# Optimization experiments

Hardware: AMD Instinct MI355X
Metric: run time of the kernel (lower is better)

## Reference

```python
import jax, jax.numpy as jnp
import numpy as np

EMBED = 1024
HEADS = 16
HEAD_DIM = EMBED // HEADS
EPS = 1e-5


def setup_inputs() -> dict:
    key = jax.random.key(0)
    ks = jax.random.split(key, 5)
    s = 1.0 / np.sqrt(EMBED)
    return {
        "x": jax.random.normal(ks[0], (2, 2048, EMBED), dtype=jnp.float32),
        "Wq": jax.random.normal(ks[1], (EMBED, EMBED), dtype=jnp.float32) * s,
        "Wk": jax.random.normal(ks[2], (EMBED, EMBED), dtype=jnp.float32) * s,
        "Wv": jax.random.normal(ks[3], (EMBED, EMBED), dtype=jnp.float32) * s,
        "Wout": jax.random.normal(ks[4], (EMBED, EMBED), dtype=jnp.float32) * s,
        "gamma": jnp.ones((EMBED,), dtype=jnp.float32),
        "beta": jnp.zeros((EMBED,), dtype=jnp.float32),
    }


def reference(x, Wq, Wk, Wv, Wout, gamma, beta):
    B, S, E = x.shape
    # nn.Linear(bias=False): y = x @ W.T; weight stored as [out, in]
    q = (x @ Wq.T).reshape(B, S, HEADS, HEAD_DIM)
    k = (x @ Wk.T).reshape(B, S, HEADS, HEAD_DIM)
    v = (x @ Wv.T).reshape(B, S, HEADS, HEAD_DIM)
    scale = 1.0 / jnp.sqrt(jnp.float32(HEAD_DIM)).astype(x.dtype)
    scores = jnp.einsum("bqhd,bkhd->bhqk", q, k) * scale  # [B,H,S,S]
    probs = jax.nn.softmax(scores, axis=-1)
    attn = jnp.einsum("bhqk,bkhd->bqhd", probs, v).reshape(B, S, E)
    out = attn @ Wout.T
    y = out + x
    mu = jnp.mean(y, axis=-1, keepdims=True)
    var = jnp.var(y, axis=-1, keepdims=True)
    return (y - mu) * jax.lax.rsqrt(var + EPS) * gamma + beta
```

## Files before the change

kernel.cpp:

```cpp
#include <hip/hip_runtime.h>
#include <hip/hip_bf16.h>
#include <cstdint>
#include <cstddef>

#define SEQ   2048
#define BATCH 2
#define NROWS 4096
#define EMB   1024
#define NHEAD 16
#define HD    64
#define KVBLK 64
#define NTG   16

typedef __attribute__((ext_vector_type(8))) short bf16x8;
typedef __attribute__((ext_vector_type(4))) float f32x4;
typedef __attribute__((ext_vector_type(16))) float f32x16;
typedef __attribute__((ext_vector_type(2))) int i32x2;
typedef __hip_bfloat16 bf16_t;

__device__ __forceinline__ int swz(int row, int cb) { return cb ^ ((row & 7) << 4); }

__device__ __forceinline__ void plswap(int a, int b, int& ra, int& rb) {
#if __has_builtin(__builtin_amdgcn_permlane32_swap)
  i32x2 r = __builtin_amdgcn_permlane32_swap(a, b, false, false);
  ra = r[0]; rb = r[1];
#else
  const int pa = __shfl_xor(a, 32), pb = __shfl_xor(b, 32);
  const bool lo = (threadIdx.x & 63) < 32;
  ra = lo ? a : pb;
  rb = lo ? pa : b;
#endif
}
__device__ __forceinline__ float pairmax32(float v) {
  int r0, r1;
  plswap(__float_as_int(v), __float_as_int(v), r0, r1);
  return fmaxf(__int_as_float(r0), __int_as_float(r1));
}
__device__ __forceinline__ float pairsum32(float v) {
  int r0, r1;
  plswap(__float_as_int(v), __float_as_int(v), r0, r1);
  return __int_as_float(r0) + __int_as_float(r1);
}

__global__ __launch_bounds__(256) void cast_f32_to_bf16(const float* __restrict__ in,
                                                        bf16_t* __restrict__ out, int n4) {
  int i = blockIdx.x * 256 + threadIdx.x;
  if (i >= n4) return;
  float4 v = reinterpret_cast<const float4*>(in)[i];
  union { ushort4 u; bf16_t h[4]; } o;
  o.h[0] = __float2bfloat16(v.x);
  o.h[1] = __float2bfloat16(v.y);
  o.h[2] = __float2bfloat16(v.z);
  o.h[3] = __float2bfloat16(v.w);
  reinterpret_cast<ushort4*>(out)[i] = o.u;
}

__global__ __launch_bounds__(256) void cast4_w(const float* __restrict__ a,
                                               const float* __restrict__ b,
                                               const float* __restrict__ c,
                                               const float* __restrict__ d,
                                               bf16_t* __restrict__ oa, bf16_t* __restrict__ ob,
                                               bf16_t* __restrict__ oc, bf16_t* __restrict__ od,
                                               int n4) {
  const int z = blockIdx.z;
  const float* in = (z == 0) ? a : (z == 1) ? b : (z == 2) ? c : d;
  bf16_t* out = (z == 0) ? oa : (z == 1) ? ob : (z == 2) ? oc : od;
  int i = blockIdx.x * 256 + threadIdx.x;
  if (i >= n4) return;
  float4 v = reinterpret_cast<const float4*>(in)[i];
  union { ushort4 u; bf16_t h[4]; } o;
  o.h[0] = __float2bfloat16(v.x);
  o.h[1] = __float2bfloat16(v.y);
  o.h[2] = __float2bfloat16(v.z);
  o.h[3] = __float2bfloat16(v.w);
  reinterpret_cast<ushort4*>(out)[i] = o.u;
}

template <int MODE>
__device__ __forceinline__ void gemm128_body(const bf16_t* __restrict__ A,
                                             const bf16_t* __restrict__ W,
                                             bf16_t* __restrict__ Ob,
                                             float* __restrict__ Of,
                                             const float* __restrict__ Res) {
  __shared__ __align__(16) bf16_t As[128 * 32];
  __shared__ __align__(16) bf16_t Bs[128 * 32];
  const int tid = threadIdx.x;
  const int lane = tid & 63;
  const int wv = tid >> 6;
  const int wm = wv >> 1, wn = wv & 1;
  const int brow = blockIdx.y * 128;
  const int bcol = blockIdx.x * 128;
  const int lr = lane & 15, lg = lane >> 4;

  f32x4 acc[4][4] = {};

  auto* As3 = (__attribute__((address_space(3))) char*)As;
  auto* Bs3 = (__attribute__((address_space(3))) char*)Bs;

  for (int k0 = 0; k0 < EMB; k0 += 32) {
    __syncthreads();
#pragma unroll
    for (int i = 0; i < 2; ++i) {
      const int chunk = i * 256 + tid;
      const int row = chunk >> 2;
      const int kc = (chunk & 3) * 8;
      const bf16_t* ga = A + (size_t)(brow + row) * EMB + k0 + kc;
      const bf16_t* gb = W + (size_t)(bcol + row) * EMB + k0 + kc;
      __builtin_amdgcn_global_load_lds((const __attribute__((address_space(1))) void*)ga,
                                       (__attribute__((address_space(3))) void*)(As3 + chunk * 16),
                                       16, 0, 0);
      __builtin_amdgcn_global_load_lds((const __attribute__((address_space(1))) void*)gb,
                                       (__attribute__((address_space(3))) void*)(Bs3 + chunk * 16),
                                       16, 0, 0);
    }
    __syncthreads();

    bf16x8 af[4], bfr[4];
#pragma unroll
    for (int m = 0; m < 4; ++m)
      af[m] = *reinterpret_cast<const bf16x8*>(&As[(wm * 64 + m * 16 + lr) * 32 + lg * 8]);
#pragma unroll
    for (int n = 0; n < 4; ++n)
      bfr[n] = *reinterpret_cast<const bf16x8*>(&Bs[(wn * 64 + n * 16 + lr) * 32 + lg * 8]);
#pragma unroll
    for (int m = 0; m < 4; ++m)
#pragma unroll
      for (int n = 0; n < 4; ++n)
        acc[m][n] = __builtin_amdgcn_mfma_f32_16x16x32_bf16(af[m], bfr[n], acc[m][n], 0, 0, 0);
  }

  const int r0 = brow + wm * 64;
  const int c0 = bcol + wn * 64;
#pragma unroll
  for (int m = 0; m < 4; ++m)
#pragma unroll
    for (int n = 0; n < 4; ++n) {
      if (MODE == 2) {
        const int row0 = r0 + m * 16 + lg * 4;
        const int col = c0 + n * 16 + lr;
        const size_t vt_row = (size_t)(row0 >> 11) * 1024 + col;
        const int s = row0 & 2047;
        union { uint2 u2; bf16_t h[4]; } pu;
#pragma unroll
        for (int r = 0; r < 4; ++r) pu.h[r] = __float2bfloat16(acc[m][n][r]);
        *reinterpret_cast<uint2*>(Ob + vt_row * SEQ + s) = pu.u2;
      } else {
#pragma unroll
        for (int r = 0; r < 4; ++r) {
          const int row = r0 + m * 16 + lg * 4 + r;
          const int col = c0 + n * 16 + lr;
          const size_t idx = (size_t)row * EMB + col;
          if (MODE == 0) Ob[idx] = __float2bfloat16(acc[m][n][r]);
          else Of[idx] = acc[m][n][r] + Res[idx];
        }
      }
    }
}

__global__ __launch_bounds__(256) void gemm_qkv(const bf16_t* __restrict__ X,
                                                const bf16_t* __restrict__ Wq,
                                                const bf16_t* __restrict__ Wk,
                                                const bf16_t* __restrict__ Wv,
                                                bf16_t* __restrict__ Q,
                                                bf16_t* __restrict__ K,
                                                bf16_t* __restrict__ Vt) {
  if (blockIdx.z == 0)      gemm128_body<0>(X, Wq, Q, nullptr, nullptr);
  else if (blockIdx.z == 1) gemm128_body<0>(X, Wk, K, nullptr, nullptr);
  else                      gemm128_body<2>(X, Wv, Vt, nullptr, nullptr);
}

__global__ __launch_bounds__(256) void gemm_out(const bf16_t* __restrict__ Attn,
                                                const bf16_t* __restrict__ Wo,
                                                float* __restrict__ Y,
                                                const float* __restrict__ X) {
  gemm128_body<1>(Attn, Wo, nullptr, Y, X);
}

__global__ __launch_bounds__(512, 4) void attn_kernel(const bf16_t* __restrict__ Q,
                                                      const bf16_t* __restrict__ K,
                                                      const bf16_t* __restrict__ Vt,
                                                      bf16_t* __restrict__ Oout) {
  __shared__ __align__(16) char L[65536];

  const int tid = threadIdx.x;
  const int lane = tid & 63;
  const int wv = tid >> 6;
  const int w = wv & 3;
  const int sg = wv >> 2;
  const int lq = lane & 31;
  const int lh = lane >> 5;

  const int f = blockIdx.x + 16 * blockIdx.y + 256 * blockIdx.z;
  const int ww = (f & 7) * 64 + (f >> 3);
  const int qb = ww & 15;
  const int h = (ww >> 4) & 15;
  const int b = ww >> 8;

  const size_t baseRow = (size_t)b * SEQ;
  const int hoff = h * HD;
  const int q0 = qb * 128 + w * 32;

  const float qscale = 0.125f * 1.44269504f;
  bf16x8 qf[4];
#pragma unroll
  for (int ks = 0; ks < 4; ++ks) {
    bf16x8 t = *reinterpret_cast<const bf16x8*>(
        &Q[(baseRow + q0 + lq) * EMB + hoff + ks * 16 + lh * 8]);
    union { bf16x8 v; bf16_t h[8]; } u;
    u.v = t;
#pragma unroll
    for (int e = 0; e < 8; ++e)
      u.h[e] = __float2bfloat16(__bfloat162float(u.h[e]) * qscale);
    qf[ks] = u.v;
  }

  f32x16 o0 = {}, o1 = {};
  float mrow = -1e30f, lrow = 0.f;

  auto* L3 = (__attribute__((address_space(3))) char*)L;
  const int gbase = sg * 32768;

  const int stid = tid & 255;
  const int srow = stid >> 3;
  const int scb = swz(srow, (stid & 7) * 16) >> 1;
  const bf16_t* kp = K + (baseRow + sg * 1024 + srow) * EMB + hoff + scb;
  const bf16_t* vp = Vt + ((size_t)(b * 1024 + hoff) + srow) * SEQ + sg * 1024 + scb;

  auto stage = [&](int buf) {
#pragma unroll
    for (int i = 0; i < 2; ++i) {
      const int c = i * 256 + stid;
      __builtin_amdgcn_global_load_lds(
          (const __attribute__((address_space(1))) void*)(kp + i * 32 * EMB),
          (__attribute__((address_space(3))) void*)(L3 + gbase + buf * 8192 + c * 16), 16, 0, 0);
      __builtin_amdgcn_global_load_lds(
          (const __attribute__((address_space(1))) void*)(vp + i * 32 * SEQ),
          (__attribute__((address_space(3))) void*)(L3 + gbase + 16384 + buf * 8192 + c * 16), 16, 0, 0);
    }
    kp += KVBLK * EMB;
    vp += KVBLK;
  };

  stage(0);
  __syncthreads();

  for (int t = 0; t < NTG; ++t) {
    const int cur = t & 1;
    if (t + 1 < NTG) stage(cur ^ 1);

    const char* Kb = (const char*)L + gbase + cur * 8192;
    const char* Vb = (const char*)L + gbase + 16384 + cur * 8192;

    f32x16 st0 = {}, st1 = {};
    __builtin_amdgcn_s_setprio(1);
#pragma unroll
    for (int ks = 0; ks < 4; ++ks) {
      bf16x8 kf0 = *reinterpret_cast<const bf16x8*>(Kb + lq * 128 + swz(lq, ks * 32 + lh * 16));
      st0 = __builtin_amdgcn_mfma_f32_32x32x16_bf16(kf0, qf[ks], st0, 0, 0, 0);
    }
#pragma unroll
    for (int ks = 0; ks < 4; ++ks) {
      bf16x8 kf1 = *reinterpret_cast<const bf16x8*>(Kb + (32 + lq) * 128 + swz(lq, ks * 32 + lh * 16));
      st1 = __builtin_amdgcn_mfma_f32_32x32x16_bf16(kf1, qf[ks], st1, 0, 0, 0);
    }
    __builtin_amdgcn_s_setprio(0);

    float mx = -1e30f;
#pragma unroll
    for (int r = 0; r < 16; ++r) mx = fmaxf(mx, st0[r]);
#pragma unroll
    for (int r = 0; r < 16; ++r) mx = fmaxf(mx, st1[r]);
    mx = pairmax32(mx);

    if (!__all(mx - mrow <= 8.f)) {
      const float mnew = fmaxf(mrow, mx);
      const float al = __builtin_amdgcn_exp2f(mrow - mnew);
      mrow = mnew;
      lrow *= al;
#pragma unroll
      for (int r = 0; r < 16; ++r) o0[r] *= al;
#pragma unroll
      for (int r = 0; r < 16; ++r) o1[r] *= al;
    }

#pragma unroll
    for (int r = 0; r < 16; ++r) st0[r] = __builtin_amdgcn_exp2f(st0[r] - mrow);
#pragma unroll
    for (int r = 0; r < 16; ++r) st1[r] = __builtin_amdgcn_exp2f(st1[r] - mrow);
    {
      float a0 = (st0[0] + st0[1]) + (st0[2] + st0[3]);
      float a1 = (st0[4] + st0[5]) + (st0[6] + st0[7]);
      float a2 = (st0[8] + st0[9]) + (st0[10] + st0[11]);
      float a3 = (st0[12] + st0[13]) + (st0[14] + st0[15]);
      float b0 = (st1[0] + st1[1]) + (st1[2] + st1[3]);
      float b1 = (st1[4] + st1[5]) + (st1[6] + st1[7]);
      float b2 = (st1[8] + st1[9]) + (st1[10] + st1[11]);
      float b3 = (st1[12] + st1[13]) + (st1[14] + st1[15]);
      lrow += pairsum32(((a0 + a1) + (a2 + a3)) + ((b0 + b1) + (b2 + b3)));
    }

    bf16x8 pb[4];
#pragma unroll
    for (int jh = 0; jh < 2; ++jh)
#pragma unroll
      for (int sub = 0; sub < 2; ++sub) {
        const f32x16& s = jh ? st1 : st0;
        int w01, w23, w45, w67;
        asm("v_cvt_pk_bf16_f32 %0, %1, %2" : "=v"(w01) : "v"(s[sub * 8 + 0]), "v"(s[sub * 8 + 1]));
        asm("v_cvt_pk_bf16_f32 %0, %1, %2" : "=v"(w23) : "v"(s[sub * 8 + 2]), "v"(s[sub * 8 + 3]));
        asm("v_cvt_pk_bf16_f32 %0, %1, %2" : "=v"(w45) : "v"(s[sub * 8 + 4]), "v"(s[sub * 8 + 5]));
        asm("v_cvt_pk_bf16_f32 %0, %1, %2" : "=v"(w67) : "v"(s[sub * 8 + 6]), "v"(s[sub * 8 + 7]));
        int d0, d1, d2, d3;
        plswap(w01, w45, d0, d2);
        plswap(w23, w67, d1, d3);
        union { int i[4]; bf16x8 v; } u;
        u.i[0] = d0; u.i[1] = d1; u.i[2] = d2; u.i[3] = d3;
        pb[jh * 2 + sub] = u.v;
      }

    __builtin_amdgcn_s_setprio(1);
#pragma unroll
    for (int js = 0; js < 4; ++js) {
      bf16x8 vf0 = *reinterpret_cast<const bf16x8*>(Vb + lq * 128 + swz(lq, js * 32 + lh * 16));
      o0 = __builtin_amdgcn_mfma_f32_32x32x16_bf16(vf0, pb[js], o0, 0, 0, 0);
    }
#pragma unroll
    for (int js = 0; js < 4; ++js) {
      bf16x8 vf1 = *reinterpret_cast<const bf16x8*>(Vb + (32 + lq) * 128 + swz(lq, js * 32 + lh * 16));
      o1 = __builtin_amdgcn_mfma_f32_32x32x16_bf16(vf1, pb[js], o1, 0, 0, 0);
    }
    __builtin_amdgcn_s_setprio(0);

    __syncthreads();
  }

  float* OL = reinterpret_cast<float*>(L + 32768);
  float2* MLx = reinterpret_cast<float2*>(L);
  __syncthreads();
  if (sg == 1) {
    MLx[w * 64 + lane] = make_float2(mrow, lrow);
#pragma unroll
    for (int r = 0; r < 16; ++r) OL[w * 2048 + r * 64 + lane] = o0[r];
#pragma unroll
    for (int r = 0; r < 16; ++r) OL[w * 2048 + (16 + r) * 64 + lane] = o1[r];
  }
  __syncthreads();
  if (sg == 0) {
    const float2 ml1 = MLx[w * 64 + lane];
    const float M = fmaxf(mrow, ml1.x);
    const float f0 = __builtin_amdgcn_exp2f(mrow - M);
    const float f1 = __builtin_amdgcn_exp2f(ml1.x - M);
    const float inv = 1.f / (f0 * lrow + f1 * ml1.y);
    const size_t orow = (baseRow + q0 + lq) * EMB + hoff;
#pragma unroll
    for (int g = 0; g < 4; ++g) {
      union { uint2 u2; bf16_t h[4]; } pu;
#pragma unroll
      for (int r = 0; r < 4; ++r)
        pu.h[r] = __float2bfloat16((f0 * o0[g * 4 + r] + f1 * OL[w * 2048 + (g * 4 + r) * 64 + lane]) * inv);
      *reinterpret_cast<uint2*>(Oout + orow + g * 8 + lh * 4) = pu.u2;
    }
#pragma unroll
    for (int g = 0; g < 4; ++g) {
      union { uint2 u2; bf16_t h[4]; } pu;
#pragma unroll
      for (int r = 0; r < 4; ++r)
        pu.h[r] = __float2bfloat16((f0 * o1[g * 4 + r] + f1 * OL[w * 2048 + (16 + g * 4 + r) * 64 + lane]) * inv);
      *reinterpret_cast<uint2*>(Oout + orow + 32 + g * 8 + lh * 4) = pu.u2;
    }
  }
}

__global__ __launch_bounds__(256) void ln_kernel(const float* __restrict__ Y,
                                                 const float* __restrict__ gamma,
                                                 const float* __restrict__ beta,
                                                 float* __restrict__ Out) {
  const int row = blockIdx.x;
  const int tid = threadIdx.x;
  const float4 v = reinterpret_cast<const float4*>(Y + (size_t)row * EMB)[tid];
  float s = v.x + v.y + v.z + v.w;
  float s2 = v.x * v.x + v.y * v.y + v.z * v.z + v.w * v.w;
#pragma unroll
  for (int m = 1; m < 64; m <<= 1) {
    s += __shfl_xor(s, m);
    s2 += __shfl_xor(s2, m);
  }
  __shared__ float ws[4], ws2[4];
  const int w = tid >> 6;
  if ((tid & 63) == 0) { ws[w] = s; ws2[w] = s2; }
  __syncthreads();
  s = ws[0] + ws[1] + ws[2] + ws[3];
  s2 = ws2[0] + ws2[1] + ws2[2] + ws2[3];
  const float mu = s * (1.f / EMB);
  const float var = s2 * (1.f / EMB) - mu * mu;
  const float rstd = rsqrtf(var + 1e-5f);
  const float4 g = reinterpret_cast<const float4*>(gamma)[tid];
  const float4 bt = reinterpret_cast<const float4*>(beta)[tid];
  float4 ov;
  ov.x = (v.x - mu) * rstd * g.x + bt.x;
  ov.y = (v.y - mu) * rstd * g.y + bt.y;
  ov.z = (v.z - mu) * rstd * g.z + bt.z;
  ov.w = (v.w - mu) * rstd * g.w + bt.w;
  reinterpret_cast<float4*>(Out + (size_t)row * EMB)[tid] = ov;
}

extern "C" void kernel_launch(void* const* d_in, const int* in_sizes, int n_in,
                              void* d_out, int out_size, void* d_ws, size_t ws_size,
                              hipStream_t stream) {
  const float* x = (const float*)d_in[0];
  const float* Wq = (const float*)d_in[1];
  const float* Wk = (const float*)d_in[2];
  const float* Wv = (const float*)d_in[3];
  const float* Wo = (const float*)d_in[4];
  const float* gamma = (const float*)d_in[5];
  const float* beta = (const float*)d_in[6];
  float* out = (float*)d_out;

  char* p = (char*)d_ws;
  const size_t sz_rows_bf = (size_t)NROWS * EMB * sizeof(bf16_t);
  const size_t sz_w_bf = (size_t)EMB * EMB * sizeof(bf16_t);
  bf16_t* xb = (bf16_t*)p; p += sz_rows_bf;
  bf16_t* wqb = (bf16_t*)p; p += sz_w_bf;
  bf16_t* wkb = (bf16_t*)p; p += sz_w_bf;
  bf16_t* wvb = (bf16_t*)p; p += sz_w_bf;
  bf16_t* wob = (bf16_t*)p; p += sz_w_bf;
  bf16_t* q = (bf16_t*)p; p += sz_rows_bf;
  bf16_t* k = (bf16_t*)p; p += sz_rows_bf;
  bf16_t* vt = (bf16_t*)p; p += sz_rows_bf;
  bf16_t* attn = (bf16_t*)p; p += sz_rows_bf;
  float* y = (float*)q;

  const int n4x = NROWS * EMB / 4;
  const int n4w = EMB * EMB / 4;
  cast_f32_to_bf16<<<n4x / 256, 256, 0, stream>>>(x, xb, n4x);
  cast4_w<<<dim3(n4w / 256, 1, 4), 256, 0, stream>>>(Wq, Wk, Wv, Wo, wqb, wkb, wvb, wob, n4w);

  gemm_qkv<<<dim3(EMB / 128, NROWS / 128, 3), 256, 0, stream>>>(xb, wqb, wkb, wvb, q, k, vt);

  attn_kernel<<<dim3(16, 16, BATCH), 512, 0, stream>>>(q, k, vt, attn);

  gemm_out<<<dim3(EMB / 128, NROWS / 128, 1), 256, 0, stream>>>(attn, wob, y, x);

  ln_kernel<<<NROWS, 256, 0, stream>>>(y, gamma, beta, out);
}
```

Measured before the change: 123.3 us.

## Rewrite QKV GEMM with 256x256 tiles, double-buffered swizzled LDS pipeline

Replaces the 128x128, single-buffered QKV projection GEMM with a 512-thread, 256x256 tile kernel. It uses K=64 steps, XOR-swizzled LDS, and double buffering with direct global-to-LDS loads interleaved between four MFMA quadrants. Explicit vmcnt/lgkmcnt waits, raw barriers and setprio aim to overlap memory traffic with matrix math and raise arithmetic intensity. The trade-offs are fewer blocks (192), which may underfill the 256 CUs, and 128KB of LDS per block with fragile hand-written synchronisation.

Measured after the change: 134.0 us. 1.09x slower.

```diff
diff --git a/kernel.cpp b/kernel.cpp
--- a/kernel.cpp
+++ b/kernel.cpp
@@ -17,6 +17,11 @@
 typedef __attribute__((ext_vector_type(16))) float f32x16;
 typedef __attribute__((ext_vector_type(2))) int i32x2;
 typedef __hip_bfloat16 bf16_t;
+
+#define RAW_BAR() do { asm volatile("" ::: "memory"); __builtin_amdgcn_s_barrier(); asm volatile("" ::: "memory"); } while (0)
+#define VMCNT6()  asm volatile("s_waitcnt vmcnt(6)" ::: "memory")
+#define VMCNT0()  asm volatile("s_waitcnt vmcnt(0)" ::: "memory")
+#define LGK0_SB() do { asm volatile("s_waitcnt lgkmcnt(0)" ::: "memory"); __builtin_amdgcn_sched_barrier(0); } while (0)
 
 __device__ __forceinline__ int swz(int row, int cb) { return cb ^ ((row & 7) << 4); }
 
@@ -76,12 +81,181 @@
   reinterpret_cast<ushort4*>(out)[i] = o.u;
 }
 
-template <int MODE>
-__device__ __forceinline__ void gemm128_body(const bf16_t* __restrict__ A,
-                                             const bf16_t* __restrict__ W,
-                                             bf16_t* __restrict__ Ob,
-                                             float* __restrict__ Of,
-                                             const float* __restrict__ Res) {
+__global__ __launch_bounds__(512) void gemm_qkv(const bf16_t* __restrict__ X,
+                                                const bf16_t* __restrict__ Wq,
+                                                const bf16_t* __restrict__ Wk,
+                                                const bf16_t* __restrict__ Wv,
+                                                bf16_t* __restrict__ Q,
+                                                bf16_t* __restrict__ K,
+                                                bf16_t* __restrict__ Vt) {
+  __shared__ __align__(16) bf16_t LA[2][256 * 64];
+  __shared__ __align__(16) bf16_t LB[2][256 * 64];
+  const int z = blockIdx.z;
+  const bf16_t* A = X;
+  const bf16_t* W = (z == 0) ? Wq : (z == 1) ? Wk : Wv;
+  bf16_t* Ob = (z == 0) ? Q : (z == 1) ? K : Vt;
+  const bool vtmode = (z == 2);
+
+  const int tid = threadIdx.x;
+  const int lane = tid & 63;
+  const int wv = tid >> 6;
+  const int wm = wv >> 2, wn = wv & 3;
+  const int brow = blockIdx.y * 256;
+  const int bcol = blockIdx.x * 256;
+  const int lr = lane & 15, lg = lane >> 4;
+
+  f32x4 acc[8][4] = {};
+
+  auto* LA3 = (__attribute__((address_space(3))) char*)&LA[0][0];
+  auto* LB3 = (__attribute__((address_space(3))) char*)&LB[0][0];
+
+  const int srow = tid >> 3;
+  const int sdst = (tid & 7) * 16;
+  const int scol = (sdst ^ ((srow & 7) << 4)) >> 1;
+  const bf16_t* Abase = A + (size_t)(brow + srow) * EMB + scol;
+  const bf16_t* Wbase = W + (size_t)(bcol + srow) * EMB + scol;
+
+  auto stageA = [&](int buf, int t, int h) {
+#pragma unroll
+    for (int i = 0; i < 2; ++i)
+      __builtin_amdgcn_global_load_lds(
+          (const __attribute__((address_space(1))) void*)(Abase + (size_t)(h * 128 + i * 64) * EMB + t * 64),
+          (__attribute__((address_space(3))) void*)(LA3 + buf * 32768 + h * 16384 + i * 8192 + tid * 16),
+          16, 0, 0);
+  };
+  auto stageB = [&](int buf, int t, int h) {
+#pragma unroll
+    for (int i = 0; i < 2; ++i)
+      __builtin_amdgcn_global_load_lds(
+          (const __attribute__((address_space(1))) void*)(Wbase + (size_t)(h * 128 + i * 64) * EMB + t * 64),
+          (__attribute__((address_space(3))) void*)(LB3 + buf * 32768 + h * 16384 + i * 8192 + tid * 16),
+          16, 0, 0);
+  };
+
+  stageA(0, 0, 0); stageA(0, 0, 1); stageB(0, 0, 0); stageB(0, 0, 1);
+  stageB(1, 1, 0); stageA(1, 1, 0); stageA(1, 1, 1);
+  VMCNT6();
+  RAW_BAR();
+
+  const char* LAc = (const char*)LA;
+  const char* LBc = (const char*)LB;
+
+  for (int t = 0; t < 16; ++t) {
+    const int buf = t & 1;
+    const char* La = LAc + buf * 32768;
+    const char* Lb = LBc + buf * 32768;
+
+    bf16x8 afr[4][2], b01[2][2], b23[2][2], afr2[4][2];
+
+    if (t + 1 < 16) stageB(buf ^ 1, t + 1, 1);
+#pragma unroll
+    for (int m = 0; m < 4; ++m)
+#pragma unroll
+      for (int kk = 0; kk < 2; ++kk)
+        afr[m][kk] = *reinterpret_cast<const bf16x8*>(
+            La + (wm * 128 + m * 16 + lr) * 128 + swz(lr, kk * 64 + lg * 16));
+#pragma unroll
+    for (int n = 0; n < 2; ++n)
+#pragma unroll
+      for (int kk = 0; kk < 2; ++kk)
+        b01[n][kk] = *reinterpret_cast<const bf16x8*>(
+            Lb + (wn * 64 + n * 16 + lr) * 128 + swz(lr, kk * 64 + lg * 16));
+    RAW_BAR();
+    LGK0_SB();
+    __builtin_amdgcn_s_setprio(1);
+#pragma unroll
+    for (int m = 0; m < 4; ++m)
+#pragma unroll
+      for (int n = 0; n < 2; ++n)
+#pragma unroll
+        for (int kk = 0; kk < 2; ++kk)
+          acc[m][n] = __builtin_amdgcn_mfma_f32_16x16x32_bf16(afr[m][kk], b01[n][kk], acc[m][n], 0, 0, 0);
+    __builtin_amdgcn_s_setprio(0);
+    RAW_BAR();
+
+#pragma unroll
+    for (int n = 0; n < 2; ++n)
+#pragma unroll
+      for (int kk = 0; kk < 2; ++kk)
+        b23[n][kk] = *reinterpret_cast<const bf16x8*>(
+            Lb + (wn * 64 + 32 + n * 16 + lr) * 128 + swz(lr, kk * 64 + lg * 16));
+    RAW_BAR();
+    LGK0_SB();
+    __builtin_amdgcn_s_setprio(1);
+#pragma unroll
+    for (int m = 0; m < 4; ++m)
+#pragma unroll
+      for (int n = 0; n < 2; ++n)
+#pragma unroll
+        for (int kk = 0; kk < 2; ++kk)
+          acc[m][n + 2] = __builtin_amdgcn_mfma_f32_16x16x32_bf16(afr[m][kk], b23[n][kk], acc[m][n + 2], 0, 0, 0);
+    __builtin_amdgcn_s_setprio(0);
+    RAW_BAR();
+
+    if (t + 2 < 16) stageB(buf, t + 2, 0);
+#pragma unroll
+    for (int m = 0; m < 4; ++m)
+#pragma unroll
+      for (int kk = 0; kk < 2; ++kk)
+        afr2[m][kk] = *reinterpret_cast<const bf16x8*>(
+            La + (wm * 128 + 64 + m * 16 + lr) * 128 + swz(lr, kk * 64 + lg * 16));
+    RAW_BAR();
+    LGK0_SB();
+    __builtin_amdgcn_s_setprio(1);
+#pragma unroll
+    for (int m = 0; m < 4; ++m)
+#pragma unroll
+      for (int n = 0; n < 2; ++n)
+#pragma unroll
+        for (int kk = 0; kk < 2; ++kk)
+          acc[m + 4][n + 2] = __builtin_amdgcn_mfma_f32_16x16x32_bf16(afr2[m][kk], b23[n][kk], acc[m + 4][n + 2], 0, 0, 0);
+    __builtin_amdgcn_s_setprio(0);
+    RAW_BAR();
+
+    if (t + 2 < 16) { stageA(buf, t + 2, 0); stageA(buf, t + 2, 1); }
+    __builtin_amdgcn_s_setprio(1);
+#pragma unroll
+    for (int m = 0; m < 4; ++m)
+#pragma unroll
+      for (int n = 0; n < 2; ++n)
+#pragma unroll
+        for (int kk = 0; kk < 2; ++kk)
+          acc[m + 4][n] = __builtin_amdgcn_mfma_f32_16x16x32_bf16(afr2[m][kk], b01[n][kk], acc[m + 4][n], 0, 0, 0);
+    __builtin_amdgcn_s_setprio(0);
+    if (t < 14) { VMCNT6(); } else { VMCNT0(); }
+    RAW_BAR();
+  }
+
+  const int r0 = brow + wm * 128;
+  const int c0 = bcol + wn * 64;
+#pragma unroll
+  for (int m = 0; m < 8; ++m)
+#pragma unroll
+    for (int n = 0; n < 4; ++n) {
+      if (vtmode) {
+        const int row0 = r0 + m * 16 + lg * 4;
+        const int col = c0 + n * 16 + lr;
+        const size_t vt_row = (size_t)(row0 >> 11) * 1024 + col;
+        const int s = row0 & 2047;
+        union { uint2 u2; bf16_t h[4]; } pu;
+#pragma unroll
+        for (int r = 0; r < 4; ++r) pu.h[r] = __float2bfloat16(acc[m][n][r]);
+        *reinterpret_cast<uint2*>(Ob + vt_row * SEQ + s) = pu.u2;
+      } else {
+#pragma unroll
+        for (int r = 0; r < 4; ++r) {
+          const int row = r0 + m * 16 + lg * 4 + r;
+          const int col = c0 + n * 16 + lr;
+          Ob[(size_t)row * EMB + col] = __float2bfloat16(acc[m][n][r]);
+        }
+      }
+    }
+}
+
+__global__ __launch_bounds__(256) void gemm_out(const bf16_t* __restrict__ Attn,
+                                                const bf16_t* __restrict__ Wo,
+                                                float* __restrict__ Y,
+                                                const float* __restrict__ X) {
   __shared__ __align__(16) bf16_t As[128 * 32];
   __shared__ __align__(16) bf16_t Bs[128 * 32];
   const int tid = threadIdx.x;
@@ -104,8 +278,8 @@
       const int chunk = i * 256 + tid;
       const int row = chunk >> 2;
       const int kc = (chunk & 3) * 8;
-      const bf16_t* ga = A + (size_t)(brow + row) * EMB + k0 + kc;
-      const bf16_t* gb = W + (size_t)(bcol + row) * EMB + k0 + kc;
+      const bf16_t* ga = Attn + (size_t)(brow + row) * EMB + k0 + kc;
+      const bf16_t* gb = Wo + (size_t)(bcol + row) * EMB + k0 + kc;
       __builtin_amdgcn_global_load_lds((const __attribute__((address_space(1))) void*)ga,
                                        (__attribute__((address_space(3))) void*)(As3 + chunk * 16),
                                        16, 0, 0);
@@ -134,46 +308,14 @@
 #pragma unroll
   for (int m = 0; m < 4; ++m)
 #pragma unroll
-    for (int n = 0; n < 4; ++n) {
-      if (MODE == 2) {
-        const int row0 = r0 + m * 16 + lg * 4;
+    for (int n = 0; n < 4; ++n)
+#pragma unroll
+      for (int r = 0; r < 4; ++r) {
+        const int row = r0 + m * 16 + lg * 4 + r;
         const int col = c0 + n * 16 + lr;
-        const size_t vt_row = (size_t)(row0 >> 11) * 1024 + col;
-        const int s = row0 & 2047;
-        union { uint2 u2; bf16_t h[4]; } pu;
-#pragma unroll
-        for (int r = 0; r < 4; ++r) pu.h[r] = __float2bfloat16(acc[m][n][r]);
-        *reinterpret_cast<uint2*>(Ob + vt_row * SEQ + s) = pu.u2;
-      } else {
-#pragma unroll
-        for (int r = 0; r < 4; ++r) {
-          const int row = r0 + m * 16 + lg * 4 + r;
-          const int col = c0 + n * 16 + lr;
-          const size_t idx = (size_t)row * EMB + col;
-          if (MODE == 0) Ob[idx] = __float2bfloat16(acc[m][n][r]);
-          else Of[idx] = acc[m][n][r] + Res[idx];
-        }
+        const size_t idx = (size_t)row * EMB + col;
+        Y[idx] = acc[m][n][r] + X[idx];
       }
-    }
-}
-
-__global__ __launch_bounds__(256) void gemm_qkv(const bf16_t* __restrict__ X,
-                                                const bf16_t* __restrict__ Wq,
-                                                const bf16_t* __restrict__ Wk,
-                                                const bf16_t* __restrict__ Wv,
-                                                bf16_t* __restrict__ Q,
-                                                bf16_t* __restrict__ K,
-                                                bf16_t* __restrict__ Vt) {
-  if (blockIdx.z == 0)      gemm128_body<0>(X, Wq, Q, nullptr, nullptr);
-  else if (blockIdx.z == 1) gemm128_body<0>(X, Wk, K, nullptr, nullptr);
-  else                      gemm128_body<2>(X, Wv, Vt, nullptr, nullptr);
-}
-
-__global__ __launch_bounds__(256) void gemm_out(const bf16_t* __restrict__ Attn,
-                                                const bf16_t* __restrict__ Wo,
-                                                float* __restrict__ Y,
-                                                const float* __restrict__ X) {
-  gemm128_body<1>(Attn, Wo, nullptr, Y, X);
 }
 
 __global__ __launch_bounds__(512, 4) void attn_kernel(const bf16_t* __restrict__ Q,
@@ -435,7 +577,7 @@
   cast_f32_to_bf16<<<n4x / 256, 256, 0, stream>>>(x, xb, n4x);
   cast4_w<<<dim3(n4w / 256, 1, 4), 256, 0, stream>>>(Wq, Wk, Wv, Wo, wqb, wkb, wvb, wob, n4w);
 
-  gemm_qkv<<<dim3(EMB / 128, NROWS / 128, 3), 256, 0, stream>>>(xb, wqb, wkb, wvb, q, k, vt);
+  gemm_qkv<<<dim3(EMB / 256, NROWS / 256, 3), 512, 0, stream>>>(xb, wqb, wkb, wvb, q, k, vt);
 
   attn_kernel<<<dim3(16, 16, BATCH), 512, 0, stream>>>(q, k, vt, attn);
 
```
